# Optimization experiments

Measured on AMD Instinct MI355X. Metric: run time of the kernel, lower is better.

The kernel has to match this reference:

```python
import jax, jax.numpy as jnp
import numpy as np

UNITS = 512
SENSORY = 256
BATCH = 256
ODE_UNFOLDS = 6
EPSILON = 1e-8
ELAPSED_TIME = 1.0


def setup_inputs() -> dict:
    key = jax.random.key(0)
    ks = jax.random.split(key, 16)
    u = lambda k, shape, lo, hi: jax.random.uniform(k, shape, jnp.float32, lo, hi)
    pm1 = lambda k, shape: (jax.random.randint(k, shape, 0, 2).astype(jnp.float32) * 2.0 - 1.0)
    return {
        "x": jax.random.normal(ks[0], (BATCH, SENSORY), jnp.float32),
        "state": jax.random.normal(ks[1], (BATCH, UNITS), jnp.float32),
        "gleak": u(ks[2], (UNITS,), 0.001, 1.0),
        "vleak": u(ks[3], (UNITS,), -0.2, 0.2),
        "cm": u(ks[4], (UNITS,), 0.4, 0.6),
        "sigma": u(ks[5], (UNITS, UNITS), 3.0, 8.0),
        "mu": u(ks[6], (UNITS, UNITS), 0.3, 0.8),
        "w": u(ks[7], (UNITS, UNITS), 0.001, 1.0),
        "erev": pm1(ks[8], (UNITS, UNITS)),
        "sensory_sigma": u(ks[9], (SENSORY, UNITS), 3.0, 8.0),
        "sensory_mu": u(ks[10], (SENSORY, UNITS), 0.3, 0.8),
        "sensory_w": u(ks[11], (SENSORY, UNITS), 0.001, 1.0),
        "sensory_erev": pm1(ks[12], (SENSORY, UNITS)),
        "input_w": jnp.ones((SENSORY,), jnp.float32),
        "input_b": jnp.zeros((SENSORY,), jnp.float32),
        "output_w": jnp.ones((UNITS,), jnp.float32),
        "output_b": jnp.zeros((UNITS,), jnp.float32),
    }


def _gate(v_pre, mu, sigma):
    # v_pre: (B, P) broadcast against (P, Q) params -> (B, P, Q)
    return jax.nn.sigmoid(sigma * (v_pre[:, :, None] - mu))


def reference(x, state, gleak, vleak, cm, sigma, mu, w, erev,
              sensory_sigma, sensory_mu, sensory_w, sensory_erev,
              input_w, input_b, output_w, output_b):
    inputs = x * input_w + input_b  # (B, D)
    sens_act = sensory_w * _gate(inputs, sensory_mu, sensory_sigma)  # (B, D, N)
    w_num_sensory = jnp.sum(sens_act * sensory_erev, axis=1)  # (B, N)
    w_den_sensory = jnp.sum(sens_act, axis=1)                 # (B, N)

    cm_t = cm / ((ELAPSED_TIME + 0.001) / ODE_UNFOLDS)  # (N,)
    v_pre = state
    for _ in range(ODE_UNFOLDS):
        w_act = w * _gate(v_pre, mu, sigma)               # (B, N, N)
        w_num = jnp.sum(w_act * erev, axis=1) + w_num_sensory
        w_den = jnp.sum(w_act, axis=1) + w_den_sensory
        numerator = cm_t * v_pre + gleak * vleak + w_num
        denominator = cm_t + gleak + w_den
        v_pre = numerator / (denominator + EPSILON)

    outputs = v_pre * output_w + output_b
    return outputs, v_pre
```

## Files before the change

kernel.cpp:

```cpp
#include <hip/hip_runtime.h>

#define UNITS 512
#define SENSD 256
#define BATCH 256
#define BN (BATCH * UNITS)
#define LOG2E 1.44269504088896340736f
#define CMF (6.0f / 1.001f)

__device__ __forceinline__ float frcp(float x)  { return __builtin_amdgcn_rcpf(x); }
__device__ __forceinline__ float fexp2(float x) { return __builtin_amdgcn_exp2f(x); }

__global__ __launch_bounds__(256) void prep_kernel(
    const float* __restrict__ sigma, const float* __restrict__ mu,
    const float* __restrict__ w, const float* __restrict__ erev,
    const float* __restrict__ ssig, const float* __restrict__ smu,
    const float* __restrict__ sw, const float* __restrict__ serev,
    const float* __restrict__ gleak, const float* __restrict__ vleak,
    const float* __restrict__ cm,
    float4* __restrict__ fusedR, float4* __restrict__ fusedS,
    float4* __restrict__ cmg) {
  int idx = blockIdx.x * 256 + threadIdx.x;
  if (idx < UNITS * UNITS) {
    float s = sigma[idx], m = mu[idx], ww = w[idx], e = erev[idx];
    fusedR[idx] = make_float4(-s * LOG2E, s * m * LOG2E, ww, ww * e);
  } else {
    int j = idx - UNITS * UNITS;
    if (j < SENSD * UNITS) {
      float s = ssig[j], m = smu[j], ww = sw[j], e = serev[j];
      fusedS[j] = make_float4(-s * LOG2E, s * m * LOG2E, ww, ww * e);
    }
  }
  if (idx < UNITS) {
    float cmt = cm[idx] * CMF, gl = gleak[idx];
    cmg[idx] = make_float4(cmt, gl * vleak[idx], cmt + gl + 1e-8f, 0.f);
  }
}

__global__ __launch_bounds__(256) void sensory_kernel(
    const float* __restrict__ x, const float* __restrict__ in_w, const float* __restrict__ in_b,
    const float4* __restrict__ fusedS,
    float* __restrict__ snf, float* __restrict__ sdf) {
  __shared__ float xl[8][128];
  int bi = blockIdx.x;
  int phs = bi & 1, qt = (bi >> 1) & 7, bt = bi >> 4;
  int tid = threadIdx.x;
  for (int i = tid; i < 1024; i += 256) {
    int br = i >> 7, dl = i & 127;
    int d = phs * 128 + dl;
    xl[br][dl] = fmaf(x[(bt * 8 + br) * SENSD + d], in_w[d], in_b[d]);
  }
  __syncthreads();
  int ql = tid & 63, bg = tid >> 6;
  int q = qt * 64 + ql;
  int r0 = bg * 2;
  const float4* F = fusedS + (size_t)(phs * 128) * UNITS + q;
  float n0 = 0.f, dn0 = 0.f, n1 = 0.f, dn1 = 0.f;
  #pragma unroll 8
  for (int dd = 0; dd < 128; ++dd) {
    float4 f = F[(size_t)dd * UNITS];
    float v0 = xl[r0][dd], v1 = xl[r0 + 1][dd];
    float t0 = fexp2(fmaf(f.x, v0, f.y));
    float t1 = fexp2(fmaf(f.x, v1, f.y));
    float s0 = frcp(1.0f + t0);
    float s1 = frcp(1.0f + t1);
    n0 = fmaf(f.w, s0, n0);  dn0 = fmaf(f.z, s0, dn0);
    n1 = fmaf(f.w, s1, n1);  dn1 = fmaf(f.z, s1, dn1);
  }
  int bp0 = (bt * 8 + r0) * UNITS + q;
  size_t o = (size_t)phs * BN + bp0;
  snf[o] = n0;         sdf[o] = dn0;
  snf[o + UNITS] = n1; sdf[o + UNITS] = dn1;
}

__global__ __launch_bounds__(256, 4) void unfold_kernel(
    const float4* __restrict__ fusedR, const float* __restrict__ vprev,
    const float* __restrict__ pn_in, const float* __restrict__ pd_in,
    const float* __restrict__ snf, const float* __restrict__ sdf,
    const float4* __restrict__ cmg,
    float* __restrict__ vout,
    float* __restrict__ pn_out, float* __restrict__ pd_out,
    int first) {
  __shared__ float vl[64][20];
  int bi = blockIdx.x;
  int ph = bi & 7, qt = (bi >> 3) & 7, bt = bi >> 6;
  int tid = threadIdx.x;
  if (first) {
    for (int i = tid; i < 1024; i += 256) {
      int br = i >> 6, pl = i & 63;
      vl[pl][br] = vprev[(bt * 16 + br) * UNITS + ph * 64 + pl];
    }
  } else {
    for (int i = tid; i < 1024; i += 256) {
      int br = i >> 6, pl = i & 63;
      int p = ph * 64 + pl;
      int bp = (bt * 16 + br) * UNITS + p;
      float num = ((pn_in[bp] + pn_in[BN + bp]) + (pn_in[2 * BN + bp] + pn_in[3 * BN + bp]))
                + ((pn_in[4 * BN + bp] + pn_in[5 * BN + bp]) + (pn_in[6 * BN + bp] + pn_in[7 * BN + bp]))
                + (snf[bp] + snf[BN + bp]);
      float den = ((pd_in[bp] + pd_in[BN + bp]) + (pd_in[2 * BN + bp] + pd_in[3 * BN + bp]))
                + ((pd_in[4 * BN + bp] + pd_in[5 * BN + bp]) + (pd_in[6 * BN + bp] + pd_in[7 * BN + bp]))
                + (sdf[bp] + sdf[BN + bp]);
      float4 c = cmg[p];
      float v = fmaf(c.x, vprev[bp], c.y + num) * frcp(c.z + den);
      vl[pl][br] = v;
      if (qt == 0) vout[bp] = v;
    }
  }
  __syncthreads();
  int ql = tid & 63, bg = tid >> 6;
  int q = qt * 64 + ql;
  int r0 = bg * 4;
  const float4* F = fusedR + (size_t)(ph * 64) * UNITS + q;
  float n0 = 0.f, n1 = 0.f, n2 = 0.f, n3 = 0.f;
  float d0 = 0.f, d1 = 0.f, d2 = 0.f, d3 = 0.f;
  #pragma unroll 8
  for (int pp = 0; pp < 64; ++pp) {
    float4 f = F[(size_t)pp * UNITS];
    float4 vv = *(const float4*)&vl[pp][r0];
    float t0 = fexp2(fmaf(f.x, vv.x, f.y));
    float t1 = fexp2(fmaf(f.x, vv.y, f.y));
    float t2 = fexp2(fmaf(f.x, vv.z, f.y));
    float t3 = fexp2(fmaf(f.x, vv.w, f.y));
    float s0 = frcp(1.0f + t0);
    float s1 = frcp(1.0f + t1);
    float s2 = frcp(1.0f + t2);
    float s3 = frcp(1.0f + t3);
    n0 = fmaf(f.w, s0, n0);  d0 = fmaf(f.z, s0, d0);
    n1 = fmaf(f.w, s1, n1);  d1 = fmaf(f.z, s1, d1);
    n2 = fmaf(f.w, s2, n2);  d2 = fmaf(f.z, s2, d2);
    n3 = fmaf(f.w, s3, n3);  d3 = fmaf(f.z, s3, d3);
  }
  int bp = (bt * 16 + r0) * UNITS + q;
  size_t o = (size_t)ph * BN + bp;
  pn_out[o] = n0;             pd_out[o] = d0;
  pn_out[o + UNITS] = n1;     pd_out[o + UNITS] = d1;
  pn_out[o + 2 * UNITS] = n2; pd_out[o + 2 * UNITS] = d2;
  pn_out[o + 3 * UNITS] = n3; pd_out[o + 3 * UNITS] = d3;
}

__global__ __launch_bounds__(256) void final_kernel(
    const float* __restrict__ vprev,
    const float* __restrict__ pn, const float* __restrict__ pd,
    const float* __restrict__ snf, const float* __restrict__ sdf,
    const float4* __restrict__ cmg,
    const float* __restrict__ ow, const float* __restrict__ ob,
    float* __restrict__ out) {
  int idx = blockIdx.x * 256 + threadIdx.x;
  if (idx >= BN) return;
  int p = idx & (UNITS - 1);
  float num = ((pn[idx] + pn[BN + idx]) + (pn[2 * BN + idx] + pn[3 * BN + idx]))
            + ((pn[4 * BN + idx] + pn[5 * BN + idx]) + (pn[6 * BN + idx] + pn[7 * BN + idx]))
            + (snf[idx] + snf[BN + idx]);
  float den = ((pd[idx] + pd[BN + idx]) + (pd[2 * BN + idx] + pd[3 * BN + idx]))
            + ((pd[4 * BN + idx] + pd[5 * BN + idx]) + (pd[6 * BN + idx] + pd[7 * BN + idx]))
            + (sdf[idx] + sdf[BN + idx]);
  float4 c = cmg[p];
  float v = fmaf(c.x, vprev[idx], c.y + num) * frcp(c.z + den);
  out[idx] = fmaf(v, ow[p], ob[p]);
  out[BN + idx] = v;
}

extern "C" void kernel_launch(void* const* d_in, const int* in_sizes, int n_in,
                              void* d_out, int out_size, void* d_ws, size_t ws_size,
                              hipStream_t stream) {
  (void)in_sizes; (void)n_in; (void)out_size; (void)ws_size;
  const float* x     = (const float*)d_in[0];
  const float* state = (const float*)d_in[1];
  const float* gleak = (const float*)d_in[2];
  const float* vleak = (const float*)d_in[3];
  const float* cm    = (const float*)d_in[4];
  const float* sigma = (const float*)d_in[5];
  const float* mu    = (const float*)d_in[6];
  const float* w     = (const float*)d_in[7];
  const float* erev  = (const float*)d_in[8];
  const float* ssig  = (const float*)d_in[9];
  const float* smu   = (const float*)d_in[10];
  const float* sw    = (const float*)d_in[11];
  const float* serev = (const float*)d_in[12];
  const float* in_w  = (const float*)d_in[13];
  const float* in_b  = (const float*)d_in[14];
  const float* out_w = (const float*)d_in[15];
  const float* out_b = (const float*)d_in[16];

  float* ws = (float*)d_ws;
  float4* fusedR = (float4*)(ws);
  float4* fusedS = (float4*)(ws + 1048576);
  float4* cmg    = (float4*)(ws + 1572864);
  float*  pnA    = ws + 1574912;
  float*  pdA    = ws + 2623488;
  float*  pnB    = ws + 3672064;
  float*  pdB    = ws + 4720640;
  float*  snf    = ws + 5769216;
  float*  sdf    = ws + 6031360;
  float*  vA     = ws + 6293504;
  float*  vB     = ws + 6424576;

  prep_kernel<<<1536, 256, 0, stream>>>(sigma, mu, w, erev, ssig, smu, sw, serev,
                                        gleak, vleak, cm, fusedR, fusedS, cmg);
  sensory_kernel<<<512, 256, 0, stream>>>(x, in_w, in_b, fusedS, snf, sdf);

  unfold_kernel<<<1024, 256, 0, stream>>>(fusedR, state, pnA, pdA, snf, sdf, cmg,
                                          vA, pnA, pdA, 1);
  unfold_kernel<<<1024, 256, 0, stream>>>(fusedR, state, pnA, pdA, snf, sdf, cmg,
                                          vA, pnB, pdB, 0);
  unfold_kernel<<<1024, 256, 0, stream>>>(fusedR, vA, pnB, pdB, snf, sdf, cmg,
                                          vB, pnA, pdA, 0);
  unfold_kernel<<<1024, 256, 0, stream>>>(fusedR, vB, pnA, pdA, snf, sdf, cmg,
                                          vA, pnB, pdB, 0);
  unfold_kernel<<<1024, 256, 0, stream>>>(fusedR, vA, pnB, pdB, snf, sdf, cmg,
                                          vB, pnA, pdA, 0);
  unfold_kernel<<<1024, 256, 0, stream>>>(fusedR, vB, pnA, pdA, snf, sdf, cmg,
                                          vA, pnB, pdB, 0);
  final_kernel<<<512, 256, 0, stream>>>(vA, pnB, pdB, snf, sdf, cmg,
                                        out_w, out_b, (float*)d_out);
}
```

Measured before the change: 158.2 us.

## Fuse six ODE unfold launches into one cooperative kernel with grid sync

Replaces the chain of six unfold kernels plus the final kernel with a single cooperative launch that loops over steps and uses grid.sync between them. Each step's state reduction from partial sums is done in-block into shared memory, which removes launch gaps and per-launch ramp-up. It needs all 1024 blocks resident at once (four per CU), and each grid barrier plus the thread fences adds synchronisation cost. It falls back to the old multi-kernel path if occupancy or the cooperative launch fails.

After: 158.5 us. About the same (+0.2%).

```diff
diff --git a/kernel.cpp b/kernel.cpp
--- a/kernel.cpp
+++ b/kernel.cpp
@@ -1,4 +1,7 @@
 #include <hip/hip_runtime.h>
+#include <hip/hip_cooperative_groups.h>
+
+namespace cg = cooperative_groups;
 
 #define UNITS 512
 #define SENSD 256
@@ -160,6 +163,108 @@
   out[BN + idx] = v;
 }
 
+__global__ __launch_bounds__(256, 4) void fused_unfold_kernel(
+    const float4* __restrict__ fusedR,
+    const float* __restrict__ state,
+    const float* __restrict__ snf, const float* __restrict__ sdf,
+    const float4* __restrict__ cmg,
+    float* __restrict__ pnA, float* __restrict__ pdA,
+    float* __restrict__ pnB, float* __restrict__ pdB,
+    float* __restrict__ vA, float* __restrict__ vB,
+    const float* __restrict__ ow, const float* __restrict__ ob,
+    float* __restrict__ out) {
+  __shared__ float vl[64][20];
+  cg::grid_group grid = cg::this_grid();
+  int bi = blockIdx.x;
+  int ph = bi & 7, qt = (bi >> 3) & 7, bt = bi >> 6;
+  int tid = threadIdx.x;
+  int ql = tid & 63, bg = tid >> 6;
+  int q = qt * 64 + ql;
+  int r0 = bg * 4;
+  const float4* F = fusedR + (size_t)(ph * 64) * UNITS + q;
+  int bpq = (bt * 16 + r0) * UNITS + q;
+
+  for (int step = 0; step < 6; ++step) {
+    const float* pn_in = (step & 1) ? pnA : pnB;
+    const float* pd_in = (step & 1) ? pdA : pdB;
+    float* pn_out = (step & 1) ? pnB : pnA;
+    float* pd_out = (step & 1) ? pdB : pdA;
+    const float* vprev = (step < 2) ? state : ((step & 1) ? vB : vA);
+    float* vout = (step & 1) ? vA : vB;
+
+    if (step == 0) {
+      for (int i = tid; i < 1024; i += 256) {
+        int br = i >> 6, pl = i & 63;
+        vl[pl][br] = state[(bt * 16 + br) * UNITS + ph * 64 + pl];
+      }
+    } else {
+      for (int i = tid; i < 1024; i += 256) {
+        int br = i >> 6, pl = i & 63;
+        int p = ph * 64 + pl;
+        int bp = (bt * 16 + br) * UNITS + p;
+        float num = ((pn_in[bp] + pn_in[BN + bp]) + (pn_in[2 * BN + bp] + pn_in[3 * BN + bp]))
+                  + ((pn_in[4 * BN + bp] + pn_in[5 * BN + bp]) + (pn_in[6 * BN + bp] + pn_in[7 * BN + bp]))
+                  + (snf[bp] + snf[BN + bp]);
+        float den = ((pd_in[bp] + pd_in[BN + bp]) + (pd_in[2 * BN + bp] + pd_in[3 * BN + bp]))
+                  + ((pd_in[4 * BN + bp] + pd_in[5 * BN + bp]) + (pd_in[6 * BN + bp] + pd_in[7 * BN + bp]))
+                  + (sdf[bp] + sdf[BN + bp]);
+        float4 c = cmg[p];
+        float v = fmaf(c.x, vprev[bp], c.y + num) * frcp(c.z + den);
+        vl[pl][br] = v;
+        if (qt == 0) vout[bp] = v;
+      }
+    }
+    __syncthreads();
+
+    float n0 = 0.f, n1 = 0.f, n2 = 0.f, n3 = 0.f;
+    float d0 = 0.f, d1 = 0.f, d2 = 0.f, d3 = 0.f;
+    #pragma unroll 8
+    for (int pp = 0; pp < 64; ++pp) {
+      float4 f = F[(size_t)pp * UNITS];
+      float4 vv = *(const float4*)&vl[pp][r0];
+      float t0 = fexp2(fmaf(f.x, vv.x, f.y));
+      float t1 = fexp2(fmaf(f.x, vv.y, f.y));
+      float t2 = fexp2(fmaf(f.x, vv.z, f.y));
+      float t3 = fexp2(fmaf(f.x, vv.w, f.y));
+      float s0 = frcp(1.0f + t0);
+      float s1 = frcp(1.0f + t1);
+      float s2 = frcp(1.0f + t2);
+      float s3 = frcp(1.0f + t3);
+      n0 = fmaf(f.w, s0, n0);  d0 = fmaf(f.z, s0, d0);
+      n1 = fmaf(f.w, s1, n1);  d1 = fmaf(f.z, s1, d1);
+      n2 = fmaf(f.w, s2, n2);  d2 = fmaf(f.z, s2, d2);
+      n3 = fmaf(f.w, s3, n3);  d3 = fmaf(f.z, s3, d3);
+    }
+    size_t o = (size_t)ph * BN + bpq;
+    pn_out[o] = n0;             pd_out[o] = d0;
+    pn_out[o + UNITS] = n1;     pd_out[o + UNITS] = d1;
+    pn_out[o + 2 * UNITS] = n2; pd_out[o + 2 * UNITS] = d2;
+    pn_out[o + 3 * UNITS] = n3; pd_out[o + 3 * UNITS] = d3;
+
+    __threadfence();
+    grid.sync();
+    __threadfence();
+  }
+
+  if (qt == 0) {
+    for (int i = tid; i < 1024; i += 256) {
+      int br = i >> 6, pl = i & 63;
+      int p = ph * 64 + pl;
+      int idx = (bt * 16 + br) * UNITS + p;
+      float num = ((pnB[idx] + pnB[BN + idx]) + (pnB[2 * BN + idx] + pnB[3 * BN + idx]))
+                + ((pnB[4 * BN + idx] + pnB[5 * BN + idx]) + (pnB[6 * BN + idx] + pnB[7 * BN + idx]))
+                + (snf[idx] + snf[BN + idx]);
+      float den = ((pdB[idx] + pdB[BN + idx]) + (pdB[2 * BN + idx] + pdB[3 * BN + idx]))
+                + ((pdB[4 * BN + idx] + pdB[5 * BN + idx]) + (pdB[6 * BN + idx] + pdB[7 * BN + idx]))
+                + (sdf[idx] + sdf[BN + idx]);
+      float4 c = cmg[p];
+      float v = fmaf(c.x, vA[idx], c.y + num) * frcp(c.z + den);
+      out[idx] = fmaf(v, ow[p], ob[p]);
+      out[BN + idx] = v;
+    }
+  }
+}
+
 extern "C" void kernel_launch(void* const* d_in, const int* in_sizes, int n_in,
                               void* d_out, int out_size, void* d_ws, size_t ws_size,
                               hipStream_t stream) {
@@ -199,18 +304,39 @@
                                         gleak, vleak, cm, fusedR, fusedS, cmg);
   sensory_kernel<<<512, 256, 0, stream>>>(x, in_w, in_b, fusedS, snf, sdf);
 
-  unfold_kernel<<<1024, 256, 0, stream>>>(fusedR, state, pnA, pdA, snf, sdf, cmg,
-                                          vA, pnA, pdA, 1);
-  unfold_kernel<<<1024, 256, 0, stream>>>(fusedR, state, pnA, pdA, snf, sdf, cmg,
-                                          vA, pnB, pdB, 0);
-  unfold_kernel<<<1024, 256, 0, stream>>>(fusedR, vA, pnB, pdB, snf, sdf, cmg,
-                                          vB, pnA, pdA, 0);
-  unfold_kernel<<<1024, 256, 0, stream>>>(fusedR, vB, pnA, pdA, snf, sdf, cmg,
-                                          vA, pnB, pdB, 0);
-  unfold_kernel<<<1024, 256, 0, stream>>>(fusedR, vA, pnB, pdB, snf, sdf, cmg,
-                                          vB, pnA, pdA, 0);
-  unfold_kernel<<<1024, 256, 0, stream>>>(fusedR, vB, pnA, pdA, snf, sdf, cmg,
-                                          vA, pnB, pdB, 0);
-  final_kernel<<<512, 256, 0, stream>>>(vA, pnB, pdB, snf, sdf, cmg,
-                                        out_w, out_b, (float*)d_out);
-}
+  int maxb = 0;
+  hipError_t occ_err = hipOccupancyMaxActiveBlocksPerMultiprocessor(
+      &maxb, (const void*)fused_unfold_kernel, 256, 0);
+  bool try_coop = (occ_err == hipSuccess && maxb >= 4);
+
+  bool coop_done = false;
+  if (try_coop) {
+    float* outp = (float*)d_out;
+    void* kargs[] = {
+      (void*)&fusedR, (void*)&state, (void*)&snf, (void*)&sdf, (void*)&cmg,
+      (void*)&pnA, (void*)&pdA, (void*)&pnB, (void*)&pdB,
+      (void*)&vA, (void*)&vB, (void*)&out_w, (void*)&out_b, (void*)&outp
+    };
+    hipError_t lerr = hipLaunchCooperativeKernel((void*)fused_unfold_kernel,
+                                                 dim3(1024), dim3(256),
+                                                 kargs, 0, stream);
+    coop_done = (lerr == hipSuccess);
+  }
+
+  if (!coop_done) {
+    unfold_kernel<<<1024, 256, 0, stream>>>(fusedR, state, pnA, pdA, snf, sdf, cmg,
+                                            vA, pnA, pdA, 1);
+    unfold_kernel<<<1024, 256, 0, stream>>>(fusedR, state, pnA, pdA, snf, sdf, cmg,
+                                            vA, pnB, pdB, 0);
+    unfold_kernel<<<1024, 256, 0, stream>>>(fusedR, vA, pnB, pdB, snf, sdf, cmg,
+                                            vB, pnA, pdA, 0);
+    unfold_kernel<<<1024, 256, 0, stream>>>(fusedR, vB, pnA, pdA, snf, sdf, cmg,
+                                            vA, pnB, pdB, 0);
+    unfold_kernel<<<1024, 256, 0, stream>>>(fusedR, vA, pnB, pdB, snf, sdf, cmg,
+                                            vB, pnA, pdA, 0);
+    unfold_kernel<<<1024, 256, 0, stream>>>(fusedR, vB, pnA, pdA, snf, sdf, cmg,
+                                            vA, pnB, pdB, 0);
+    final_kernel<<<512, 256, 0, stream>>>(vA, pnB, pdB, snf, sdf, cmg,
+                                          out_w, out_b, (float*)d_out);
+  }
+}
```

## Retile unfold kernel to 16 p-splits and 32 batch rows per block

Applied to the files above, without the earlier changes.

The unfold kernel's tiling changes from 8 presynaptic splits of 64 with 16 batch rows per block to 16 splits of 32 with 32 batch rows. Each thread now accumulates 8 batch rows instead of 4, so every fusedR float4 load is reused across twice as many sigmoid evaluations. In exchange, the partial-sum buffers double to 16 slices. Every next unfold and the final kernel must read and reduce 16 partials instead of 8, which adds global traffic and workspace. Register pressure also rises with 16 accumulators.

New measurement: 165.9 us. 4.9% more time.

```diff
diff --git a/kernel.cpp b/kernel.cpp
--- a/kernel.cpp
+++ b/kernel.cpp
@@ -80,26 +80,28 @@
     float* __restrict__ vout,
     float* __restrict__ pn_out, float* __restrict__ pd_out,
     int first) {
-  __shared__ float vl[64][20];
+  __shared__ float vl[32][40];
   int bi = blockIdx.x;
-  int ph = bi & 7, qt = (bi >> 3) & 7, bt = bi >> 6;
+  int ph = bi & 15, qt = (bi >> 4) & 7, bt = bi >> 7;
   int tid = threadIdx.x;
   if (first) {
     for (int i = tid; i < 1024; i += 256) {
-      int br = i >> 6, pl = i & 63;
-      vl[pl][br] = vprev[(bt * 16 + br) * UNITS + ph * 64 + pl];
+      int br = i >> 5, pl = i & 31;
+      vl[pl][br] = vprev[(bt * 32 + br) * UNITS + ph * 32 + pl];
     }
   } else {
     for (int i = tid; i < 1024; i += 256) {
-      int br = i >> 6, pl = i & 63;
-      int p = ph * 64 + pl;
-      int bp = (bt * 16 + br) * UNITS + p;
-      float num = ((pn_in[bp] + pn_in[BN + bp]) + (pn_in[2 * BN + bp] + pn_in[3 * BN + bp]))
-                + ((pn_in[4 * BN + bp] + pn_in[5 * BN + bp]) + (pn_in[6 * BN + bp] + pn_in[7 * BN + bp]))
-                + (snf[bp] + snf[BN + bp]);
-      float den = ((pd_in[bp] + pd_in[BN + bp]) + (pd_in[2 * BN + bp] + pd_in[3 * BN + bp]))
-                + ((pd_in[4 * BN + bp] + pd_in[5 * BN + bp]) + (pd_in[6 * BN + bp] + pd_in[7 * BN + bp]))
-                + (sdf[bp] + sdf[BN + bp]);
+      int br = i >> 5, pl = i & 31;
+      int p = ph * 32 + pl;
+      int bp = (bt * 32 + br) * UNITS + p;
+      float num = 0.f, den = 0.f;
+      #pragma unroll
+      for (int k = 0; k < 16; ++k) {
+        num += pn_in[k * BN + bp];
+        den += pd_in[k * BN + bp];
+      }
+      num += snf[bp] + snf[BN + bp];
+      den += sdf[bp] + sdf[BN + bp];
       float4 c = cmg[p];
       float v = fmaf(c.x, vprev[bp], c.y + num) * frcp(c.z + den);
       vl[pl][br] = v;
@@ -109,33 +111,52 @@
   __syncthreads();
   int ql = tid & 63, bg = tid >> 6;
   int q = qt * 64 + ql;
-  int r0 = bg * 4;
-  const float4* F = fusedR + (size_t)(ph * 64) * UNITS + q;
+  int r0 = bg * 8;
+  const float4* F = fusedR + (size_t)(ph * 32) * UNITS + q;
   float n0 = 0.f, n1 = 0.f, n2 = 0.f, n3 = 0.f;
+  float n4 = 0.f, n5 = 0.f, n6 = 0.f, n7 = 0.f;
   float d0 = 0.f, d1 = 0.f, d2 = 0.f, d3 = 0.f;
-  #pragma unroll 8
-  for (int pp = 0; pp < 64; ++pp) {
+  float d4 = 0.f, d5 = 0.f, d6 = 0.f, d7 = 0.f;
+  #pragma unroll 4
+  for (int pp = 0; pp < 32; ++pp) {
     float4 f = F[(size_t)pp * UNITS];
-    float4 vv = *(const float4*)&vl[pp][r0];
-    float t0 = fexp2(fmaf(f.x, vv.x, f.y));
-    float t1 = fexp2(fmaf(f.x, vv.y, f.y));
-    float t2 = fexp2(fmaf(f.x, vv.z, f.y));
-    float t3 = fexp2(fmaf(f.x, vv.w, f.y));
+    float4 va = *(const float4*)&vl[pp][r0];
+    float4 vb = *(const float4*)&vl[pp][r0 + 4];
+    float t0 = fexp2(fmaf(f.x, va.x, f.y));
+    float t1 = fexp2(fmaf(f.x, va.y, f.y));
+    float t2 = fexp2(fmaf(f.x, va.z, f.y));
+    float t3 = fexp2(fmaf(f.x, va.w, f.y));
+    float t4 = fexp2(fmaf(f.x, vb.x, f.y));
+    float t5 = fexp2(fmaf(f.x, vb.y, f.y));
+    float t6 = fexp2(fmaf(f.x, vb.z, f.y));
+    float t7 = fexp2(fmaf(f.x, vb.w, f.y));
     float s0 = frcp(1.0f + t0);
     float s1 = frcp(1.0f + t1);
     float s2 = frcp(1.0f + t2);
     float s3 = frcp(1.0f + t3);
+    float s4 = frcp(1.0f + t4);
+    float s5 = frcp(1.0f + t5);
+    float s6 = frcp(1.0f + t6);
+    float s7 = frcp(1.0f + t7);
     n0 = fmaf(f.w, s0, n0);  d0 = fmaf(f.z, s0, d0);
     n1 = fmaf(f.w, s1, n1);  d1 = fmaf(f.z, s1, d1);
     n2 = fmaf(f.w, s2, n2);  d2 = fmaf(f.z, s2, d2);
     n3 = fmaf(f.w, s3, n3);  d3 = fmaf(f.z, s3, d3);
-  }
-  int bp = (bt * 16 + r0) * UNITS + q;
+    n4 = fmaf(f.w, s4, n4);  d4 = fmaf(f.z, s4, d4);
+    n5 = fmaf(f.w, s5, n5);  d5 = fmaf(f.z, s5, d5);
+    n6 = fmaf(f.w, s6, n6);  d6 = fmaf(f.z, s6, d6);
+    n7 = fmaf(f.w, s7, n7);  d7 = fmaf(f.z, s7, d7);
+  }
+  int bp = (bt * 32 + r0) * UNITS + q;
   size_t o = (size_t)ph * BN + bp;
   pn_out[o] = n0;             pd_out[o] = d0;
   pn_out[o + UNITS] = n1;     pd_out[o + UNITS] = d1;
   pn_out[o + 2 * UNITS] = n2; pd_out[o + 2 * UNITS] = d2;
   pn_out[o + 3 * UNITS] = n3; pd_out[o + 3 * UNITS] = d3;
+  pn_out[o + 4 * UNITS] = n4; pd_out[o + 4 * UNITS] = d4;
+  pn_out[o + 5 * UNITS] = n5; pd_out[o + 5 * UNITS] = d5;
+  pn_out[o + 6 * UNITS] = n6; pd_out[o + 6 * UNITS] = d6;
+  pn_out[o + 7 * UNITS] = n7; pd_out[o + 7 * UNITS] = d7;
 }
 
 __global__ __launch_bounds__(256) void final_kernel(
@@ -148,12 +169,14 @@
   int idx = blockIdx.x * 256 + threadIdx.x;
   if (idx >= BN) return;
   int p = idx & (UNITS - 1);
-  float num = ((pn[idx] + pn[BN + idx]) + (pn[2 * BN + idx] + pn[3 * BN + idx]))
-            + ((pn[4 * BN + idx] + pn[5 * BN + idx]) + (pn[6 * BN + idx] + pn[7 * BN + idx]))
-            + (snf[idx] + snf[BN + idx]);
-  float den = ((pd[idx] + pd[BN + idx]) + (pd[2 * BN + idx] + pd[3 * BN + idx]))
-            + ((pd[4 * BN + idx] + pd[5 * BN + idx]) + (pd[6 * BN + idx] + pd[7 * BN + idx]))
-            + (sdf[idx] + sdf[BN + idx]);
+  float num = 0.f, den = 0.f;
+  #pragma unroll
+  for (int k = 0; k < 16; ++k) {
+    num += pn[k * BN + idx];
+    den += pd[k * BN + idx];
+  }
+  num += snf[idx] + snf[BN + idx];
+  den += sdf[idx] + sdf[BN + idx];
   float4 c = cmg[p];
   float v = fmaf(c.x, vprev[idx], c.y + num) * frcp(c.z + den);
   out[idx] = fmaf(v, ow[p], ob[p]);
@@ -187,13 +210,13 @@
   float4* fusedS = (float4*)(ws + 1048576);
   float4* cmg    = (float4*)(ws + 1572864);
   float*  pnA    = ws + 1574912;
-  float*  pdA    = ws + 2623488;
-  float*  pnB    = ws + 3672064;
-  float*  pdB    = ws + 4720640;
-  float*  snf    = ws + 5769216;
-  float*  sdf    = ws + 6031360;
-  float*  vA     = ws + 6293504;
-  float*  vB     = ws + 6424576;
+  float*  pdA    = ws + 3672064;
+  float*  pnB    = ws + 5769216;
+  float*  pdB    = ws + 7866368;
+  float*  snf    = ws + 9963520;
+  float*  sdf    = ws + 10225664;
+  float*  vA     = ws + 10487808;
+  float*  vB     = ws + 10618880;
 
   prep_kernel<<<1536, 256, 0, stream>>>(sigma, mu, w, erev, ssig, smu, sw, serev,
                                         gleak, vleak, cm, fusedR, fusedS, cmg);
```
